# Optimization experiments

Hardware: AMD Instinct MI355X
Metric: run time of the kernel (lower is better)

## Reference

```python
import jax, jax.numpy as jnp
import numpy as np

N = 50000       # nodes
E = 1_600_000   # edges
IN = 128; H = 128; CLS = 128; OUT = 64; G = 128  # feature dims, num graphs
EPS = 1e-5


def setup_inputs() -> dict:
    key = jax.random.key(0)
    ks = jax.random.split(key, 8)
    def w(k, shape):
        return jax.random.normal(k, shape, jnp.float32) / np.sqrt(shape[0])
    return {
        "x": jax.random.normal(ks[0], (N, IN), jnp.float32),
        "edge_index": jax.random.randint(ks[1], (2, E), 0, N),
        "batch": jnp.sort(jax.random.randint(ks[2], (N,), 0, G)),
        "conv_w0": w(ks[3], (IN, H)), "conv_b0": jnp.zeros((H,), jnp.float32),
        "conv_w1": w(ks[4], (H, H)),  "conv_b1": jnp.zeros((H,), jnp.float32),
        "conv_w2": w(ks[5], (H, H)),  "conv_b2": jnp.zeros((H,), jnp.float32),
        "bn_g0": jnp.ones((H,), jnp.float32), "bn_b0": jnp.zeros((H,), jnp.float32),
        "bn_g1": jnp.ones((H,), jnp.float32), "bn_b1": jnp.zeros((H,), jnp.float32),
        "bn_g2": jnp.ones((H,), jnp.float32), "bn_b2": jnp.zeros((H,), jnp.float32),
        "lin1_w": w(ks[6], (H, CLS)),  "lin1_b": jnp.zeros((CLS,), jnp.float32),
        "lin2_w": w(ks[7], (CLS, OUT)), "lin2_b": jnp.zeros((OUT,), jnp.float32),
        "fc_w": w(jax.random.fold_in(key, 99), (OUT, OUT)), "fc_b": jnp.zeros((OUT,), jnp.float32),
    }


def _gcn_norm(edge_index):
    # add self-loops, compute symmetric normalization coefficients per edge
    src = jnp.concatenate([edge_index[0], jnp.arange(N)])
    dst = jnp.concatenate([edge_index[1], jnp.arange(N)])
    deg = jax.ops.segment_sum(jnp.ones_like(dst, jnp.float32), dst, num_segments=N)
    dis = jax.lax.rsqrt(jnp.maximum(deg, 1.0))  # deg >= 1 due to self-loops
    norm = dis[src] * dis[dst]                  # [E+N]
    return src, dst, norm


def _gcn_conv(x, w, b, src, dst, norm):
    h = x @ w                                   # [N, H]
    msg = h[src] * norm[:, None]                # gather  [E+N, H]
    agg = jax.ops.segment_sum(msg, dst, num_segments=N)  # scatter-add
    return agg + b


def _bn_relu(x, g, b):
    mean = jnp.mean(x, axis=0)
    var = jnp.mean(jnp.square(x - mean), axis=0)  # biased var (torch BN training)
    return jax.nn.relu((x - mean) * jax.lax.rsqrt(var + EPS) * g + b)


def reference(x, edge_index, batch,
              conv_w0, conv_b0, conv_w1, conv_b1, conv_w2, conv_b2,
              bn_g0, bn_b0, bn_g1, bn_b1, bn_g2, bn_b2,
              lin1_w, lin1_b, lin2_w, lin2_b, fc_w, fc_b):
    src, dst, norm = _gcn_norm(edge_index)
    for w, b, g, bb in ((conv_w0, conv_b0, bn_g0, bn_b0),
                        (conv_w1, conv_b1, bn_g1, bn_b1),
                        (conv_w2, conv_b2, bn_g2, bn_b2)):
        x = _bn_relu(_gcn_conv(x, w, b, src, dst, norm), g, bb)
    # global mean pool over graphs
    summed = jax.ops.segment_sum(x, batch, num_segments=G)          # [G, H]
    cnt = jax.ops.segment_sum(jnp.ones((N,), jnp.float32), batch, num_segments=G)
    pooled = summed / jnp.maximum(cnt, 1.0)[:, None]
    h = pooled @ lin1_w + lin1_b
    h = h @ lin2_w + lin2_b
    h = h @ fc_w + fc_b
    return jnp.where(h >= 0, h, 0.01 * h)  # LeakyReLU(0.01)
```

## Files before the change

### kernel.cpp

```cpp
#include <hip/hip_runtime.h>
#include <hip/hip_fp16.h>

constexpr int F      = 128;
constexpr int OUTF   = 64;
constexpr int NGRAPH = 128;
constexpr int POOL_CHUNK = 64;
constexpr int NP1    = 256;
constexpr int STAT_ROWS = 128;

using half8 = __attribute__((ext_vector_type(8))) _Float16;
using f32x4 = __attribute__((ext_vector_type(4))) float;
using f32x8 = __attribute__((ext_vector_type(8))) float;

__global__ __launch_bounds__(256) void k_scan1(const int* __restrict__ src,
                                               int* __restrict__ out, int* __restrict__ bsum, int n) {
    __shared__ int tmp[256];
    int i = blockIdx.x * 256 + threadIdx.x;
    int v = (i < n) ? src[i] : 0;
    tmp[threadIdx.x] = v;
    __syncthreads();
    for (int s = 1; s < 256; s <<= 1) {
        int t = (threadIdx.x >= s) ? tmp[threadIdx.x - s] : 0;
        __syncthreads();
        tmp[threadIdx.x] += t;
        __syncthreads();
    }
    if (i < n) out[i] = tmp[threadIdx.x] - v;
    if (threadIdx.x == 255) bsum[blockIdx.x] = tmp[255];
}

__global__ __launch_bounds__(256) void k_scan2(int* bsum, int nb) {
    __shared__ int tmp[256];
    int i = threadIdx.x;
    int v = (i < nb) ? bsum[i] : 0;
    tmp[i] = v;
    __syncthreads();
    for (int s = 1; s < 256; s <<= 1) {
        int t = (i >= s) ? tmp[i - s] : 0;
        __syncthreads();
        tmp[i] += t;
        __syncthreads();
    }
    if (i < nb) bsum[i] = tmp[i] - v;
}

__global__ __launch_bounds__(256) void k_scan3(const int* __restrict__ degi, int* __restrict__ off,
                                               const int* __restrict__ bsum, int* __restrict__ cursor, int n) {
    int i = blockIdx.x * 256 + threadIdx.x;
    if (i < n) {
        int o = off[i] + bsum[i >> 8];
        off[i] = o;
        cursor[i] = o;
        if (i == n - 1) off[n] = o + degi[i];
    }
}

__global__ __launch_bounds__(256) void k_scan3b(int* __restrict__ arr, const int* __restrict__ bsum, int n) {
    int i = blockIdx.x * 256 + threadIdx.x;
    if (i < n) arr[i] += bsum[i >> 8];
}

__global__ __launch_bounds__(256) void k_hist(const int* __restrict__ dst,
                                              int* __restrict__ histg, int e, int nbuckets) {
    __shared__ int lh[256];
    lh[threadIdx.x] = 0;
    __syncthreads();
    const int chunk = (e + NP1 - 1) / NP1;
    const int i0 = blockIdx.x * chunk;
    const int i1 = min(i0 + chunk, e);
    for (int i = i0 + threadIdx.x; i < i1; i += 256)
        atomicAdd(&lh[dst[i] >> 8], 1);
    __syncthreads();
    if (threadIdx.x < nbuckets)
        histg[threadIdx.x * NP1 + blockIdx.x] = lh[threadIdx.x];
}

__global__ __launch_bounds__(256) void k_part(const int* __restrict__ src, const int* __restrict__ dst,
                                              const int* __restrict__ hbase,
                                              unsigned* __restrict__ tmp, int e, int nbuckets) {
    __shared__ int lc[256];
    if (threadIdx.x < nbuckets)
        lc[threadIdx.x] = hbase[threadIdx.x * NP1 + blockIdx.x];
    __syncthreads();
    const int chunk = (e + NP1 - 1) / NP1;
    const int i0 = blockIdx.x * chunk;
    const int i1 = min(i0 + chunk, e);
    for (int i = i0 + threadIdx.x; i < i1; i += 256) {
        int s = src[i], d = dst[i];
        int pos = atomicAdd(&lc[d >> 8], 1);
        tmp[pos] = ((unsigned)s << 8) | (unsigned)(d & 255);
    }
}

__global__ __launch_bounds__(256) void k_degB(const unsigned* __restrict__ tmp,
                                              const int* __restrict__ hbase,
                                              int* __restrict__ degi, float* __restrict__ dis,
                                              int e, int n, int nbuckets) {
    __shared__ int lh[256];
    lh[threadIdx.x] = 0;
    __syncthreads();
    const int b = blockIdx.x;
    const int j0 = hbase[b * NP1];
    const int j1 = (b + 1 < nbuckets) ? hbase[(b + 1) * NP1] : e;
    for (int j = j0 + threadIdx.x; j < j1; j += 256)
        atomicAdd(&lh[tmp[j] & 255u], 1);
    __syncthreads();
    const int node = (b << 8) + threadIdx.x;
    if (node < n) {
        int dv = lh[threadIdx.x];
        degi[node] = dv;
        dis[node] = rsqrtf((float)(dv + 1));
    }
}

__global__ __launch_bounds__(256) void k_scatB(const unsigned* __restrict__ tmp, const int* __restrict__ off,
                                               const float* __restrict__ dis, int* __restrict__ cursor,
                                               unsigned* __restrict__ csr4, int n) {
    int n0 = blockIdx.x << 8;
    int n1 = min(n0 + 256, n);
    int j1 = off[n1];
    for (int j = off[n0] + threadIdx.x; j < j1; j += 256) {
        unsigned v = tmp[j];
        int s = (int)(v >> 8);
        int d = n0 + (int)(v & 255u);
        float nm = dis[s] * dis[d];
        int pos = atomicAdd(&cursor[d], 1);
        unsigned short nh = __builtin_bit_cast(unsigned short, (_Float16)nm);
        csr4[pos] = (unsigned)s | ((unsigned)nh << 16);
    }
}

template <typename T>
__global__ __launch_bounds__(256) void k_gemm_mfma(const T* __restrict__ in,
                                                   const float* __restrict__ w,
                                                   _Float16* __restrict__ out,
                                                   const float* __restrict__ scale,
                                                   const float* __restrict__ shift,
                                                   int n, int apply) {
    __shared__ _Float16 wt[F][F + 8];
    const int t = threadIdx.x;
#pragma unroll
    for (int r = 0; r < 64; ++r) {
        int idx = r * 256 + t;
        int k = idx >> 7, nn = idx & (F - 1);
        wt[nn][k] = (_Float16)w[idx];
    }
    __syncthreads();

    const int wave = t >> 6, lane = t & 63;
    const int row0 = blockIdx.x * 64 + wave * 16;
    const int arow = row0 + (lane & 15);
    const int kblk = (lane >> 4) * 8;
    const bool rvalid = arow < n;

    f32x4 acc[8];
#pragma unroll
    for (int nt = 0; nt < 8; ++nt) acc[nt] = (f32x4){0.f, 0.f, 0.f, 0.f};

#pragma unroll
    for (int ks = 0; ks < 4; ++ks) {
        const int k0 = ks * 32 + kblk;
        half8 afrag;
        if (rvalid) {
            float av[8];
            if constexpr (sizeof(T) == 4) {
                f32x8 v = *(const f32x8*)&in[(size_t)arow * F + k0];
#pragma unroll
                for (int i = 0; i < 8; ++i) av[i] = v[i];
            } else {
                half8 v = *(const half8*)&in[(size_t)arow * F + k0];
#pragma unroll
                for (int i = 0; i < 8; ++i) av[i] = (float)v[i];
            }
            if (apply) {
                f32x8 sc = *(const f32x8*)&scale[k0];
                f32x8 sh = *(const f32x8*)&shift[k0];
#pragma unroll
                for (int i = 0; i < 8; ++i) av[i] = fmaxf(av[i] * sc[i] + sh[i], 0.f);
            }
#pragma unroll
            for (int i = 0; i < 8; ++i) afrag[i] = (_Float16)av[i];
        } else {
#pragma unroll
            for (int i = 0; i < 8; ++i) afrag[i] = (_Float16)0.f;
        }
#pragma unroll
        for (int nt = 0; nt < 8; ++nt) {
            const half8 bfrag = *(const half8*)&wt[nt * 16 + (lane & 15)][k0];
            acc[nt] = __builtin_amdgcn_mfma_f32_16x16x32_f16(afrag, bfrag, acc[nt], 0, 0, 0);
        }
    }

    const int orow = row0 + (lane >> 4) * 4;
    const int ocol = lane & 15;
#pragma unroll
    for (int i = 0; i < 4; ++i) {
        if (orow + i < n) {
            _Float16* op = &out[(size_t)(orow + i) * F + ocol];
#pragma unroll
            for (int nt = 0; nt < 8; ++nt) op[nt * 16] = (_Float16)acc[nt][i];
        }
    }
}

__global__ __launch_bounds__(256) void k_gcn_agg(const _Float16* __restrict__ h,
                                                 const unsigned* __restrict__ csr4,
                                                 const int* __restrict__ off,
                                                 const float* __restrict__ dis,
                                                 const float* __restrict__ bias,
                                                 _Float16* __restrict__ aggh, int n) {
    const int t = threadIdx.x;
    const int node = blockIdx.x * 16 + (t >> 4);
    if (node >= n) return;
    const int f0 = (t & 15) << 3;
    float d = dis[node];
    float dd = d * d;
    const half8 hv0 = *(const half8*)&h[(size_t)node * F + f0];
    float acc[8];
#pragma unroll
    for (int i = 0; i < 8; ++i) acc[i] = (float)hv0[i] * dd + bias[f0 + i];

    int k = off[node];
    const int k1 = off[node + 1];
    for (; k + 3 < k1; k += 4) {
        unsigned u0 = __builtin_nontemporal_load(&csr4[k]);
        unsigned u1 = __builtin_nontemporal_load(&csr4[k + 1]);
        unsigned u2 = __builtin_nontemporal_load(&csr4[k + 2]);
        unsigned u3 = __builtin_nontemporal_load(&csr4[k + 3]);
        int s0 = (int)(u0 & 0xFFFFu), s1 = (int)(u1 & 0xFFFFu);
        int s2 = (int)(u2 & 0xFFFFu), s3 = (int)(u3 & 0xFFFFu);
        float nm0 = (float)__builtin_bit_cast(_Float16, (unsigned short)(u0 >> 16));
        float nm1 = (float)__builtin_bit_cast(_Float16, (unsigned short)(u1 >> 16));
        float nm2 = (float)__builtin_bit_cast(_Float16, (unsigned short)(u2 >> 16));
        float nm3 = (float)__builtin_bit_cast(_Float16, (unsigned short)(u3 >> 16));
        const half8 a = *(const half8*)&h[(size_t)s0 * F + f0];
        const half8 b = *(const half8*)&h[(size_t)s1 * F + f0];
        const half8 c = *(const half8*)&h[(size_t)s2 * F + f0];
        const half8 e = *(const half8*)&h[(size_t)s3 * F + f0];
#pragma unroll
        for (int i = 0; i < 8; ++i) acc[i] += (float)a[i] * nm0;
#pragma unroll
        for (int i = 0; i < 8; ++i) acc[i] += (float)b[i] * nm1;
#pragma unroll
        for (int i = 0; i < 8; ++i) acc[i] += (float)c[i] * nm2;
#pragma unroll
        for (int i = 0; i < 8; ++i) acc[i] += (float)e[i] * nm3;
    }
    for (; k < k1; ++k) {
        unsigned u0 = __builtin_nontemporal_load(&csr4[k]);
        int s0 = (int)(u0 & 0xFFFFu);
        float nm0 = (float)__builtin_bit_cast(_Float16, (unsigned short)(u0 >> 16));
        const half8 a = *(const half8*)&h[(size_t)s0 * F + f0];
#pragma unroll
        for (int i = 0; i < 8; ++i) acc[i] += (float)a[i] * nm0;
    }
    half8 res;
#pragma unroll
    for (int i = 0; i < 8; ++i) res[i] = (_Float16)acc[i];
    *(half8*)&aggh[(size_t)node * F + f0] = res;
}

__global__ __launch_bounds__(256) void k_stats(const _Float16* __restrict__ aggh,
                                               float* __restrict__ sum,
                                               float* __restrict__ sumsq, int n) {
    __shared__ float ls[F], lq[F];
    const int t = threadIdx.x;
    const int col = t & (F - 1);
    const int row0 = blockIdx.x * STAT_ROWS + (t >> 7);
    const int rend = min(blockIdx.x * STAT_ROWS + STAT_ROWS, n);
    float s = 0.f, q = 0.f;
    for (int r = row0; r < rend; r += 2) {
        float v = (float)aggh[(size_t)r * F + col];
        s += v; q += v * v;
    }
    if (t >= F) { ls[col] = s; lq[col] = q; }
    __syncthreads();
    if (t < F) {
        s += ls[col]; q += lq[col];
        unsafeAtomicAdd(&sum[col], s);
        unsafeAtomicAdd(&sumsq[col], q);
    }
}

__global__ __launch_bounds__(256) void k_zero(float* p, int n) {
    int i = blockIdx.x * 256 + threadIdx.x;
    if (i < n) p[i] = 0.f;
}

__global__ __launch_bounds__(128) void k_stats_final(float* __restrict__ sum,
                                                     float* __restrict__ sumsq,
                                                     const float* __restrict__ g,
                                                     const float* __restrict__ b,
                                                     float* scale, float* shift, int n) {
    int t = threadIdx.x;
    float mean = sum[t] / (float)n;
    float var = fmaxf(sumsq[t] / (float)n - mean * mean, 0.f);
    float inv = rsqrtf(var + 1e-5f);
    float sc = g[t] * inv;
    scale[t] = sc;
    shift[t] = b[t] - mean * sc;
    sum[t] = 0.f;
    sumsq[t] = 0.f;
}

__global__ __launch_bounds__(128) void k_pool(const _Float16* __restrict__ aggh,
                                              const int* __restrict__ batch,
                                              const float* __restrict__ scale,
                                              const float* __restrict__ shift,
                                              float* pooled, float* cnt, int n) {
    int t = threadIdx.x;
    int row0 = blockIdx.x * POOL_CHUNK;
    if (row0 >= n) return;
    int rend = min(row0 + POOL_CHUNK, n);
    float sc = scale[t], sh = shift[t];
    int gcur = batch[row0];
    float acc = 0.f, c = 0.f;
    for (int r = row0; r < rend; ++r) {
        int g = batch[r];
        if (g != gcur) {
            unsafeAtomicAdd(&pooled[gcur * F + t], acc);
            if (t == 0) unsafeAtomicAdd(&cnt[gcur], c);
            acc = 0.f; c = 0.f; gcur = g;
        }
        float v = fmaxf((float)aggh[(size_t)r * F + t] * sc + sh, 0.f);
        acc += v; c += 1.f;
    }
    unsafeAtomicAdd(&pooled[gcur * F + t], acc);
    if (t == 0) unsafeAtomicAdd(&cnt[gcur], c);
}

__global__ __launch_bounds__(128) void k_mlp(const float* __restrict__ pooled,
                                             const float* __restrict__ cnt,
                                             const float* __restrict__ l1w, const float* __restrict__ l1b,
                                             const float* __restrict__ l2w, const float* __restrict__ l2b,
                                             const float* __restrict__ fcw, const float* __restrict__ fcb,
                                             float* __restrict__ out) {
    __shared__ float pr[F], h1[F], h2[OUTF];
    int g = blockIdx.x, t = threadIdx.x;
    float c = fmaxf(cnt[g], 1.f);
    pr[t] = pooled[g * F + t] / c;
    __syncthreads();
    float a = l1b[t];
#pragma unroll 4
    for (int k = 0; k < F; ++k) a += pr[k] * l1w[k * F + t];
    h1[t] = a;
    __syncthreads();
    if (t < OUTF) {
        float b = l2b[t];
#pragma unroll 4
        for (int k = 0; k < F; ++k) b += h1[k] * l2w[k * OUTF + t];
        h2[t] = b;
    }
    __syncthreads();
    if (t < OUTF) {
        float o = fcb[t];
#pragma unroll 4
        for (int k = 0; k < OUTF; ++k) o += h2[k] * fcw[k * OUTF + t];
        out[g * OUTF + t] = (o >= 0.f) ? o : 0.01f * o;
    }
}

extern "C" void kernel_launch(void* const* d_in, const int* in_sizes, int n_in,
                              void* d_out, int out_size, void* d_ws, size_t ws_size,
                              hipStream_t stream) {
    const float* x      = (const float*)d_in[0];
    const int*   ei     = (const int*)d_in[1];
    const int*   batch  = (const int*)d_in[2];
    const float* convw[3] = {(const float*)d_in[3], (const float*)d_in[5], (const float*)d_in[7]};
    const float* convb[3] = {(const float*)d_in[4], (const float*)d_in[6], (const float*)d_in[8]};
    const float* bng[3]   = {(const float*)d_in[9],  (const float*)d_in[11], (const float*)d_in[13]};
    const float* bnb[3]   = {(const float*)d_in[10], (const float*)d_in[12], (const float*)d_in[14]};
    const float* l1w = (const float*)d_in[15]; const float* l1b = (const float*)d_in[16];
    const float* l2w = (const float*)d_in[17]; const float* l2b = (const float*)d_in[18];
    const float* fcw = (const float*)d_in[19]; const float* fcb = (const float*)d_in[20];

    const int N = in_sizes[2];
    const int E = in_sizes[1] / 2;
    const int* srcp = ei;
    const int* dstp = ei + E;
    const int NB = (N + 255) / 256;
    const int NBUCK = (N + 255) >> 8;
    const int HLEN = NBUCK * NP1;
    const int HB = (HLEN + 255) / 256;

    char* wsp = (char*)d_ws;
    size_t off_b = 0;
    auto alloc = [&](size_t bytes) -> void* {
        void* p = wsp + off_b;
        off_b += (bytes + 255) / 256 * 256;
        return p;
    };
    int*      degi    = (int*)alloc((size_t)N * 4);
    float*    dis     = (float*)alloc((size_t)N * 4);
    int*      offs    = (int*)alloc((size_t)(N + 1) * 4);
    int*      cursor  = (int*)alloc((size_t)N * 4);
    int*      bsum    = (int*)alloc(256 * 4);
    int*      hbase   = (int*)alloc((size_t)HLEN * 4);
    int*      bsum2   = (int*)alloc(256 * 4);
    unsigned* tmp     = (unsigned*)alloc((size_t)E * 4);
    unsigned* csr4    = (unsigned*)alloc((size_t)E * 4);
    _Float16* hbuf    = (_Float16*)alloc((size_t)N * F * 2);
    _Float16* aggh    = (_Float16*)alloc((size_t)N * F * 2);
    float*    sum     = (float*)alloc(F * 4);
    float*    sumsq   = (float*)alloc(F * 4);
    float*    scale   = (float*)alloc(F * 4);
    float*    shift   = (float*)alloc(F * 4);
    float*    pooled  = (float*)alloc(NGRAPH * F * 4);
    float*    cnt     = (float*)alloc(NGRAPH * 4);
    (void)ws_size; (void)n_in; (void)out_size;

    k_hist<<<NP1, 256, 0, stream>>>(dstp, hbase, E, NBUCK);
    k_scan1<<<HB, 256, 0, stream>>>(hbase, hbase, bsum2, HLEN);
    k_scan2<<<1, 256, 0, stream>>>(bsum2, HB);
    k_scan3b<<<HB, 256, 0, stream>>>(hbase, bsum2, HLEN);
    k_part<<<NP1, 256, 0, stream>>>(srcp, dstp, hbase, tmp, E, NBUCK);
    k_degB<<<NBUCK, 256, 0, stream>>>(tmp, hbase, degi, dis, E, N, NBUCK);

    k_scan1<<<NB, 256, 0, stream>>>(degi, offs, bsum, N);
    k_scan2<<<1, 256, 0, stream>>>(bsum, NB);
    k_scan3<<<NB, 256, 0, stream>>>(degi, offs, bsum, cursor, N);
    k_scatB<<<NBUCK, 256, 0, stream>>>(tmp, offs, dis, cursor, csr4, N);

    k_zero<<<1, 256, 0, stream>>>(sum, 2 * F);

    const int SB = (N + STAT_ROWS - 1) / STAT_ROWS;
    for (int l = 0; l < 3; ++l) {
        if (l == 0)
            k_gemm_mfma<float><<<(N + 63) / 64, 256, 0, stream>>>(
                x, convw[l], hbuf, scale, shift, N, 0);
        else
            k_gemm_mfma<_Float16><<<(N + 63) / 64, 256, 0, stream>>>(
                aggh, convw[l], hbuf, scale, shift, N, 1);
        k_gcn_agg<<<(N + 15) / 16, 256, 0, stream>>>(hbuf, csr4, offs, dis, convb[l], aggh, N);
        k_stats<<<SB, 256, 0, stream>>>(aggh, sum, sumsq, N);
        k_stats_final<<<1, 128, 0, stream>>>(sum, sumsq, bng[l], bnb[l], scale, shift, N);
    }

    k_zero<<<(NGRAPH * F + NGRAPH + 255) / 256, 256, 0, stream>>>(pooled, NGRAPH * F + NGRAPH);
    k_pool<<<(N + POOL_CHUNK - 1) / POOL_CHUNK, 128, 0, stream>>>(aggh, batch, scale, shift, pooled, cnt, N);
    k_mlp<<<NGRAPH, 128, 0, stream>>>(pooled, cnt, l1w, l1b, l2w, l2b, fcw, fcb, (float*)d_out);
}
```

Measured before the change: 529.4 us.

## Process aggregation nodes in degree-sorted order and enlarge GEMM blocks

Builds a degree histogram and a counting-sort permutation of nodes so each aggregation block handles nodes of similar degree, reducing intra-wave load imbalance. The GEMM kernel now uses 512-thread blocks covering 128 rows, amortizing the per-block weight transpose into shared memory. Adds four small setup launches, and the permuted node order gives scattered output rows.

```diff
diff --git a/kernel.cpp b/kernel.cpp
--- a/kernel.cpp
+++ b/kernel.cpp
@@ -130,8 +130,27 @@
     }
 }
 
+__global__ __launch_bounds__(256) void k_dhist(const int* __restrict__ degi, int* __restrict__ dhist, int n) {
+    __shared__ int lh[256];
+    lh[threadIdx.x] = 0;
+    __syncthreads();
+    for (int i = blockIdx.x * 256 + threadIdx.x; i < n; i += gridDim.x * 256)
+        atomicAdd(&lh[min(degi[i], 255)], 1);
+    __syncthreads();
+    if (lh[threadIdx.x]) atomicAdd(&dhist[threadIdx.x], lh[threadIdx.x]);
+}
+
+__global__ __launch_bounds__(256) void k_dscat(const int* __restrict__ degi, int* __restrict__ dcur,
+                                               int* __restrict__ order, int n) {
+    int i = blockIdx.x * 256 + threadIdx.x;
+    if (i < n) {
+        int pos = atomicAdd(&dcur[min(degi[i], 255)], 1);
+        order[pos] = i;
+    }
+}
+
 template <typename T>
-__global__ __launch_bounds__(256) void k_gemm_mfma(const T* __restrict__ in,
+__global__ __launch_bounds__(512) void k_gemm_mfma(const T* __restrict__ in,
                                                    const float* __restrict__ w,
                                                    _Float16* __restrict__ out,
                                                    const float* __restrict__ scale,
@@ -140,15 +159,15 @@
     __shared__ _Float16 wt[F][F + 8];
     const int t = threadIdx.x;
 #pragma unroll
-    for (int r = 0; r < 64; ++r) {
-        int idx = r * 256 + t;
+    for (int r = 0; r < 32; ++r) {
+        int idx = r * 512 + t;
         int k = idx >> 7, nn = idx & (F - 1);
         wt[nn][k] = (_Float16)w[idx];
     }
     __syncthreads();
 
     const int wave = t >> 6, lane = t & 63;
-    const int row0 = blockIdx.x * 64 + wave * 16;
+    const int row0 = blockIdx.x * 128 + wave * 16;
     const int arow = row0 + (lane & 15);
     const int kblk = (lane >> 4) * 8;
     const bool rvalid = arow < n;
@@ -208,10 +227,12 @@
                                                  const int* __restrict__ off,
                                                  const float* __restrict__ dis,
                                                  const float* __restrict__ bias,
+                                                 const int* __restrict__ order,
                                                  _Float16* __restrict__ aggh, int n) {
     const int t = threadIdx.x;
-    const int node = blockIdx.x * 16 + (t >> 4);
-    if (node >= n) return;
+    const int idx = blockIdx.x * 16 + (t >> 4);
+    if (idx >= n) return;
+    const int node = order[idx];
     const int f0 = (t & 15) << 3;
     float d = dis[node];
     float dd = d * d;
@@ -394,9 +415,11 @@
     float*    dis     = (float*)alloc((size_t)N * 4);
     int*      offs    = (int*)alloc((size_t)(N + 1) * 4);
     int*      cursor  = (int*)alloc((size_t)N * 4);
+    int*      order   = (int*)alloc((size_t)N * 4);
     int*      bsum    = (int*)alloc(256 * 4);
     int*      hbase   = (int*)alloc((size_t)HLEN * 4);
     int*      bsum2   = (int*)alloc(256 * 4);
+    int*      dhist   = (int*)alloc(256 * 4);
     unsigned* tmp     = (unsigned*)alloc((size_t)E * 4);
     unsigned* csr4    = (unsigned*)alloc((size_t)E * 4);
     _Float16* hbuf    = (_Float16*)alloc((size_t)N * F * 2);
@@ -421,17 +444,22 @@
     k_scan3<<<NB, 256, 0, stream>>>(degi, offs, bsum, cursor, N);
     k_scatB<<<NBUCK, 256, 0, stream>>>(tmp, offs, dis, cursor, csr4, N);
 
+    k_zero<<<1, 256, 0, stream>>>((float*)dhist, 256);
+    k_dhist<<<64, 256, 0, stream>>>(degi, dhist, N);
+    k_scan2<<<1, 256, 0, stream>>>(dhist, 256);
+    k_dscat<<<NB, 256, 0, stream>>>(degi, dhist, order, N);
+
     k_zero<<<1, 256, 0, stream>>>(sum, 2 * F);
 
     const int SB = (N + STAT_ROWS - 1) / STAT_ROWS;
     for (int l = 0; l < 3; ++l) {
         if (l == 0)
-            k_gemm_mfma<float><<<(N + 63) / 64, 256, 0, stream>>>(
+            k_gemm_mfma<float><<<(N + 127) / 128, 512, 0, stream>>>(
                 x, convw[l], hbuf, scale, shift, N, 0);
         else
-            k_gemm_mfma<_Float16><<<(N + 63) / 64, 256, 0, stream>>>(
+            k_gemm_mfma<_Float16><<<(N + 127) / 128, 512, 0, stream>>>(
                 aggh, convw[l], hbuf, scale, shift, N, 1);
-        k_gcn_agg<<<(N + 15) / 16, 256, 0, stream>>>(hbuf, csr4, offs, dis, convb[l], aggh, N);
+        k_gcn_agg<<<(N + 15) / 16, 256, 0, stream>>>(hbuf, csr4, offs, dis, convb[l], order, aggh, N);
         k_stats<<<SB, 256, 0, stream>>>(aggh, sum, sumsq, N);
         k_stats_final<<<1, 128, 0, stream>>>(sum, sumsq, bng[l], bnb[l], scale, shift, N);
     }
```

New measurement: 635.6 us. +20.1%, slower.
